# Kernel tuning notes

Hardware: AMD Instinct MI355X
Metric: run time of the kernel (lower is better)

## Reference

```python
import jax, jax.numpy as jnp
import numpy as np

PAD_IDX = 0  # y_vocab.token_to_idx('<PAD>'); source also hard-codes argmax==0 as stop
B, N, M, V, T = 8, 6, 64, 32000, 8  # N = max_span, T = template_len


def setup_inputs() -> dict:
    key = jax.random.key(0)
    k1, k2, k3 = jax.random.split(key, 3)
    input_decodings = jax.random.normal(k1, (B, N, M, V), dtype=jnp.float32)
    template = jax.random.uniform(k2, (B, T, N + 1), dtype=jnp.float32)
    spans = jax.random.randint(k3, (B,), 0, N)
    return {"input_decodings": input_decodings, "template": template, "spans": spans}


def reference(input_decodings, template, spans):
    Bq, Nq, Mq, Vq = input_decodings.shape
    Tq = template.shape[1]
    # original only reads template[i, t, :spans[i]+1]; zero out the rest
    span_mask = jnp.arange(Nq + 1)[None, None, :] <= spans[:, None, None]
    tmpl = jnp.where(span_mask, template, jnp.zeros((), template.dtype))
    # choices[b] = [pad_vector, flatten(input_decodings[b,0]), ..., flatten(input_decodings[b,N-1])]
    pad_vec = jnp.zeros((Mq * Vq,), input_decodings.dtype).at[PAD_IDX].set(1.0)
    choices = jnp.concatenate(
        [jnp.broadcast_to(pad_vec, (Bq, 1, Mq * Vq)), input_decodings.reshape(Bq, Nq, Mq * Vq)],
        axis=1,
    )  # [B, N+1, M*V]
    # all per-step template matmuls at once: [B, T, M, V]
    outputs = jnp.einsum('bts,bsd->btd', tmpl, choices).reshape(Bq, Tq, Mq, Vq)

    pos = jnp.arange(Mq)

    def step(carry, out_t):
        idx, result = carry  # idx: [B] int, result: [B, M, V]
        amax = jnp.argmax(out_t, axis=-1)  # [B, M]
        iszero = amax == 0
        # length of leading run of nonzero argmax (stop at first zero)
        out_len = jnp.where(jnp.any(iszero, axis=1), jnp.argmax(iszero, axis=1).astype(jnp.int32), Mq)
        out_len = jnp.minimum(out_len, Mq - idx)
        wmask = (pos[None, :] >= idx[:, None]) & (pos[None, :] < (idx + out_len)[:, None])  # [B, M]
        gather_idx = jnp.clip(pos[None, :] - idx[:, None], 0, Mq - 1)  # [B, M]
        src = jnp.take_along_axis(out_t, gather_idx[:, :, None], axis=1)  # [B, M, V]
        result = jnp.where(wmask[:, :, None], src, result)
        return (idx + out_len, result), None

    init = (jnp.zeros((Bq,), jnp.int32), jnp.zeros((Bq, Mq, Vq), input_decodings.dtype))
    (final_idx, result), _ = jax.lax.scan(step, init, jnp.swapaxes(outputs, 0, 1))
    return result
```

## Files before the change

### kernel.cpp

```cpp
#include <hip/hip_runtime.h>
#include <math.h>

namespace {
constexpr int kB = 8;
constexpr int kN = 6;
constexpr int kM = 64;
constexpr int kV = 32000;
constexpr int kT = 8;
constexpr int kS = kN + 1;
constexpr int kV4 = kV / 4;
constexpr int kThreads = 256;
}

__global__ void init_ws_kernel(int* __restrict__ len_raw) {
  int i = threadIdx.x;
  if (i < kB * kT) len_raw[i] = kM;
}

template <int NUSE>
__device__ __forceinline__ void pass1_body(const float* __restrict__ in,
                                           const float* __restrict__ tw,
                                           float* __restrict__ orow,
                                           int b, int m,
                                           int* __restrict__ len_raw) {
  const int tid = threadIdx.x;
  constexpr int NA = NUSE > 0 ? NUSE : 1;

  float w[kT][NA];
  float w0[kT];
#pragma unroll
  for (int t = 0; t < kT; ++t) {
    w0[t] = tw[t * kS];
#pragma unroll
    for (int n = 0; n < NUSE; ++n) w[t][n] = tw[t * kS + n + 1];
  }

  const float4* rows[NA];
#pragma unroll
  for (int n = 0; n < NUSE; ++n)
    rows[n] = (const float4*)(in + ((size_t)(b * kN + n) * kM + m) * kV);

  float mx[kT], v0[kT];
#pragma unroll
  for (int t = 0; t < kT; ++t) {
    mx[t] = -INFINITY;
    v0[t] = 0.0f;
  }

  for (int v4 = tid; v4 < kV4; v4 += kThreads) {
    float4 x[NA];
#pragma unroll
    for (int n = 0; n < NUSE; ++n) x[n] = rows[n][v4];
    const bool head = (v4 == 0);
#pragma unroll
    for (int t = 0; t < kT; ++t) {
      float ax = 0.0f, ay = 0.0f, az = 0.0f, aw = 0.0f;
#pragma unroll
      for (int n = 0; n < NUSE; ++n) {
        ax = fmaf(w[t][n], x[n].x, ax);
        ay = fmaf(w[t][n], x[n].y, ay);
        az = fmaf(w[t][n], x[n].z, az);
        aw = fmaf(w[t][n], x[n].w, aw);
      }
      if (head && m == 0) ax += w0[t];
      if (head) v0[t] = ax;
      mx[t] = fmaxf(mx[t], fmaxf(fmaxf(ax, ay), fmaxf(az, aw)));
      if (t == 0) ((float4*)orow)[v4] = make_float4(ax, ay, az, aw);
    }
  }

  __shared__ float red[kT][4];
  const int lane = tid & 63;
  const int wv = tid >> 6;
#pragma unroll
  for (int t = 0; t < kT; ++t) {
    float v = mx[t];
#pragma unroll
    for (int off = 32; off > 0; off >>= 1) v = fmaxf(v, __shfl_xor(v, off, 64));
    if (lane == 0) red[t][wv] = v;
  }
  __syncthreads();
  if (tid == 0) {
#pragma unroll
    for (int t = 0; t < kT; ++t) {
      float bm = fmaxf(fmaxf(red[t][0], red[t][1]), fmaxf(red[t][2], red[t][3]));
      if (v0[t] >= bm) atomicMin(&len_raw[b * kT + t], m);
    }
  }
}

__global__ __launch_bounds__(kThreads) void pass1_kernel(
    const float* __restrict__ in, const float* __restrict__ tmpl,
    const int* __restrict__ spans, float* __restrict__ out,
    int* __restrict__ len_raw) {
  const int blk = blockIdx.x;
  const int b = blk >> 6;
  const int m = blk & 63;
  int span = spans[b];
  int nuse = span < 0 ? 0 : (span > kN ? kN : span);
  const float* tw = tmpl + (size_t)b * kT * kS;
  float* orow = out + (size_t)(b * kM + m) * kV;
  switch (nuse) {
    case 0: pass1_body<0>(in, tw, orow, b, m, len_raw); break;
    case 1: pass1_body<1>(in, tw, orow, b, m, len_raw); break;
    case 2: pass1_body<2>(in, tw, orow, b, m, len_raw); break;
    case 3: pass1_body<3>(in, tw, orow, b, m, len_raw); break;
    case 4: pass1_body<4>(in, tw, orow, b, m, len_raw); break;
    case 5: pass1_body<5>(in, tw, orow, b, m, len_raw); break;
    case 6: pass1_body<6>(in, tw, orow, b, m, len_raw); break;
  }
}

__global__ void pass2_kernel(const int* __restrict__ len_raw,
                             int* __restrict__ sel) {
  int b = threadIdx.x;
  if (b >= kB) return;
  for (int m = 0; m < kM; ++m) sel[b * kM + m] = -1;
  int idx = 0;
  for (int t = 0; t < kT; ++t) {
    int L = len_raw[b * kT + t];
    if (L > kM - idx) L = kM - idx;
    for (int j = 0; j < L; ++j) sel[b * kM + idx + j] = t * 64 + j;
    idx += L;
  }
}

__global__ __launch_bounds__(kThreads) void pass3_kernel(
    const float* __restrict__ in, const float* __restrict__ tmpl,
    const int* __restrict__ spans, const int* __restrict__ sel,
    float* __restrict__ out) {
  const int blk = blockIdx.x;
  const int b = blk >> 6;
  const int m = blk & 63;
  const int s = sel[b * kM + m];
  if (s >= 0 && s < 64) return;

  const int tid = threadIdx.x;
  float* orow = out + (size_t)(b * kM + m) * kV;

  if (s < 0) {
    float4 z = make_float4(0.0f, 0.0f, 0.0f, 0.0f);
    for (int v4 = tid; v4 < kV4; v4 += kThreads) ((float4*)orow)[v4] = z;
    return;
  }

  const int t = s >> 6;
  const int row = s & 63;
  int span = spans[b];
  int nuse = span < 0 ? 0 : (span > kN ? kN : span);
  const float* tw = tmpl + ((size_t)b * kT + t) * kS;
  const float w0 = tw[0];
  float w[kN];
  for (int n = 0; n < kN; ++n) w[n] = (n < nuse) ? tw[n + 1] : 0.0f;

  const float4* rows[kN];
  for (int n = 0; n < kN; ++n)
    rows[n] = (const float4*)(in + ((size_t)(b * kN + n) * kM + row) * kV);

  for (int v4 = tid; v4 < kV4; v4 += kThreads) {
    float ax = 0.0f, ay = 0.0f, az = 0.0f, aw = 0.0f;
    for (int n = 0; n < nuse; ++n) {
      float4 x = rows[n][v4];
      ax = fmaf(w[n], x.x, ax);
      ay = fmaf(w[n], x.y, ay);
      az = fmaf(w[n], x.z, az);
      aw = fmaf(w[n], x.w, aw);
    }
    if (v4 == 0 && row == 0) ax += w0;
    ((float4*)orow)[v4] = make_float4(ax, ay, az, aw);
  }
}

extern "C" void kernel_launch(void* const* d_in, const int* in_sizes, int n_in,
                              void* d_out, int out_size, void* d_ws,
                              size_t ws_size, hipStream_t stream) {
  const float* in = (const float*)d_in[0];
  const float* tmpl = (const float*)d_in[1];
  const int* spans = (const int*)d_in[2];
  float* out = (float*)d_out;

  int* len_raw = (int*)d_ws;
  int* sel = len_raw + kB * kT;

  hipLaunchKernelGGL(init_ws_kernel, dim3(1), dim3(64), 0, stream, len_raw);
  hipLaunchKernelGGL(pass1_kernel, dim3(kB * kM), dim3(kThreads), 0, stream,
                     in, tmpl, spans, out, len_raw);
  hipLaunchKernelGGL(pass2_kernel, dim3(1), dim3(64), 0, stream, len_raw, sel);
  hipLaunchKernelGGL(pass3_kernel, dim3(kB * kM), dim3(kThreads), 0, stream,
                     in, tmpl, spans, sel, out);
}
```

Baseline: 506.6 us.

## Replace atomic length scan with per-row flags and merge selection into patch kernel

Pass 1 now writes a per-(batch, template step, row) flag instead of doing an atomicMin, so the init and serial pass2 kernels can be dropped. The patch kernel rebuilds each step's length with a wavefront ballot and recomputes the row selection per block. Loads and stores on the large activation and output streams become nontemporal to reduce cache pollution. This cuts two kernel launches and one serial kernel, at the cost of every patch block redundantly reading 512 flags.

```diff
diff --git a/kernel.cpp b/kernel.cpp
--- a/kernel.cpp
+++ b/kernel.cpp
@@ -12,17 +12,15 @@
 constexpr int kThreads = 256;
 }
 
-__global__ void init_ws_kernel(int* __restrict__ len_raw) {
-  int i = threadIdx.x;
-  if (i < kB * kT) len_raw[i] = kM;
-}
+typedef float f32x4 __attribute__((ext_vector_type(4)));
+
 
 template <int NUSE>
 __device__ __forceinline__ void pass1_body(const float* __restrict__ in,
                                            const float* __restrict__ tw,
                                            float* __restrict__ orow,
                                            int b, int m,
-                                           int* __restrict__ len_raw) {
+                                           int* __restrict__ flags) {
   const int tid = threadIdx.x;
   constexpr int NA = NUSE > 0 ? NUSE : 1;
 
@@ -35,10 +33,12 @@
     for (int n = 0; n < NUSE; ++n) w[t][n] = tw[t * kS + n + 1];
   }
 
-  const float4* rows[NA];
+  const f32x4* rows[NA];
 #pragma unroll
   for (int n = 0; n < NUSE; ++n)
-    rows[n] = (const float4*)(in + ((size_t)(b * kN + n) * kM + m) * kV);
+    rows[n] = (const f32x4*)(in + ((size_t)(b * kN + n) * kM + m) * kV);
+
+  f32x4* orow4 = (f32x4*)orow;
 
   float mx[kT], v0[kT];
 #pragma unroll
@@ -48,9 +48,9 @@
   }
 
   for (int v4 = tid; v4 < kV4; v4 += kThreads) {
-    float4 x[NA];
-#pragma unroll
-    for (int n = 0; n < NUSE; ++n) x[n] = rows[n][v4];
+    f32x4 x[NA];
+#pragma unroll
+    for (int n = 0; n < NUSE; ++n) x[n] = __builtin_nontemporal_load(&rows[n][v4]);
     const bool head = (v4 == 0);
 #pragma unroll
     for (int t = 0; t < kT; ++t) {
@@ -65,7 +65,10 @@
       if (head && m == 0) ax += w0[t];
       if (head) v0[t] = ax;
       mx[t] = fmaxf(mx[t], fmaxf(fmaxf(ax, ay), fmaxf(az, aw)));
-      if (t == 0) ((float4*)orow)[v4] = make_float4(ax, ay, az, aw);
+      if (t == 0) {
+        f32x4 o = {ax, ay, az, aw};
+        __builtin_nontemporal_store(o, &orow4[v4]);
+      }
     }
   }
 
@@ -84,7 +87,7 @@
 #pragma unroll
     for (int t = 0; t < kT; ++t) {
       float bm = fmaxf(fmaxf(red[t][0], red[t][1]), fmaxf(red[t][2], red[t][3]));
-      if (v0[t] >= bm) atomicMin(&len_raw[b * kT + t], m);
+      flags[(b * kT + t) * kM + m] = (v0[t] >= bm) ? 1 : 0;
     }
   }
 }
@@ -92,7 +95,7 @@
 __global__ __launch_bounds__(kThreads) void pass1_kernel(
     const float* __restrict__ in, const float* __restrict__ tmpl,
     const int* __restrict__ spans, float* __restrict__ out,
-    int* __restrict__ len_raw) {
+    int* __restrict__ flags) {
   const int blk = blockIdx.x;
   const int b = blk >> 6;
   const int m = blk & 63;
@@ -101,51 +104,63 @@
   const float* tw = tmpl + (size_t)b * kT * kS;
   float* orow = out + (size_t)(b * kM + m) * kV;
   switch (nuse) {
-    case 0: pass1_body<0>(in, tw, orow, b, m, len_raw); break;
-    case 1: pass1_body<1>(in, tw, orow, b, m, len_raw); break;
-    case 2: pass1_body<2>(in, tw, orow, b, m, len_raw); break;
-    case 3: pass1_body<3>(in, tw, orow, b, m, len_raw); break;
-    case 4: pass1_body<4>(in, tw, orow, b, m, len_raw); break;
-    case 5: pass1_body<5>(in, tw, orow, b, m, len_raw); break;
-    case 6: pass1_body<6>(in, tw, orow, b, m, len_raw); break;
-  }
-}
-
-__global__ void pass2_kernel(const int* __restrict__ len_raw,
-                             int* __restrict__ sel) {
-  int b = threadIdx.x;
-  if (b >= kB) return;
-  for (int m = 0; m < kM; ++m) sel[b * kM + m] = -1;
-  int idx = 0;
-  for (int t = 0; t < kT; ++t) {
-    int L = len_raw[b * kT + t];
-    if (L > kM - idx) L = kM - idx;
-    for (int j = 0; j < L; ++j) sel[b * kM + idx + j] = t * 64 + j;
-    idx += L;
-  }
-}
-
-__global__ __launch_bounds__(kThreads) void pass3_kernel(
+    case 0: pass1_body<0>(in, tw, orow, b, m, flags); break;
+    case 1: pass1_body<1>(in, tw, orow, b, m, flags); break;
+    case 2: pass1_body<2>(in, tw, orow, b, m, flags); break;
+    case 3: pass1_body<3>(in, tw, orow, b, m, flags); break;
+    case 4: pass1_body<4>(in, tw, orow, b, m, flags); break;
+    case 5: pass1_body<5>(in, tw, orow, b, m, flags); break;
+    case 6: pass1_body<6>(in, tw, orow, b, m, flags); break;
+  }
+}
+
+__global__ __launch_bounds__(kThreads) void patch_kernel(
     const float* __restrict__ in, const float* __restrict__ tmpl,
-    const int* __restrict__ spans, const int* __restrict__ sel,
+    const int* __restrict__ spans, const int* __restrict__ flags,
     float* __restrict__ out) {
   const int blk = blockIdx.x;
   const int b = blk >> 6;
   const int m = blk & 63;
-  const int s = sel[b * kM + m];
-  if (s >= 0 && s < 64) return;
-
   const int tid = threadIdx.x;
+  const int lane = tid & 63;
+
+  __shared__ int slen[kT];
+  if (tid < 64) {
+#pragma unroll
+    for (int t = 0; t < kT; ++t) {
+      int f = flags[(b * kT + t) * kM + lane];
+      unsigned long long bal = __ballot(f != 0);
+      if (lane == 0) slen[t] = bal ? (int)(__ffsll((long long)bal) - 1) : kM;
+    }
+  }
+  __syncthreads();
+
+  int sel_t = -1, sel_row = 0, idx = 0;
+#pragma unroll
+  for (int t = 0; t < kT; ++t) {
+    int L = slen[t];
+    if (L > kM - idx) L = kM - idx;
+    if (sel_t < 0 && m >= idx && m < idx + L) {
+      sel_t = t;
+      sel_row = m - idx;
+    }
+    idx += L;
+  }
+
+  if (sel_t == 0) return;
+
   float* orow = out + (size_t)(b * kM + m) * kV;
-
-  if (s < 0) {
-    float4 z = make_float4(0.0f, 0.0f, 0.0f, 0.0f);
-    for (int v4 = tid; v4 < kV4; v4 += kThreads) ((float4*)orow)[v4] = z;
+  f32x4* orow4 = (f32x4*)orow;
+
+  if (sel_t < 0) {
+    f32x4 z = {0.0f, 0.0f, 0.0f, 0.0f};
+    for (int v4 = tid; v4 < kV4; v4 += kThreads)
+      __builtin_nontemporal_store(z, &orow4[v4]);
     return;
   }
 
-  const int t = s >> 6;
-  const int row = s & 63;
+  const int t = sel_t;
+  const int row = sel_row;
   int span = spans[b];
   int nuse = span < 0 ? 0 : (span > kN ? kN : span);
   const float* tw = tmpl + ((size_t)b * kT + t) * kS;
@@ -153,21 +168,22 @@
   float w[kN];
   for (int n = 0; n < kN; ++n) w[n] = (n < nuse) ? tw[n + 1] : 0.0f;
 
-  const float4* rows[kN];
+  const f32x4* rows[kN];
   for (int n = 0; n < kN; ++n)
-    rows[n] = (const float4*)(in + ((size_t)(b * kN + n) * kM + row) * kV);
+    rows[n] = (const f32x4*)(in + ((size_t)(b * kN + n) * kM + row) * kV);
 
   for (int v4 = tid; v4 < kV4; v4 += kThreads) {
     float ax = 0.0f, ay = 0.0f, az = 0.0f, aw = 0.0f;
     for (int n = 0; n < nuse; ++n) {
-      float4 x = rows[n][v4];
+      f32x4 x = __builtin_nontemporal_load(&rows[n][v4]);
       ax = fmaf(w[n], x.x, ax);
       ay = fmaf(w[n], x.y, ay);
       az = fmaf(w[n], x.z, az);
       aw = fmaf(w[n], x.w, aw);
     }
     if (v4 == 0 && row == 0) ax += w0;
-    ((float4*)orow)[v4] = make_float4(ax, ay, az, aw);
+    f32x4 o = {ax, ay, az, aw};
+    __builtin_nontemporal_store(o, &orow4[v4]);
   }
 }
 
@@ -179,13 +195,10 @@
   const int* spans = (const int*)d_in[2];
   float* out = (float*)d_out;
 
-  int* len_raw = (int*)d_ws;
-  int* sel = len_raw + kB * kT;
-
-  hipLaunchKernelGGL(init_ws_kernel, dim3(1), dim3(64), 0, stream, len_raw);
+  int* flags = (int*)d_ws;
+
   hipLaunchKernelGGL(pass1_kernel, dim3(kB * kM), dim3(kThreads), 0, stream,
-                     in, tmpl, spans, out, len_raw);
-  hipLaunchKernelGGL(pass2_kernel, dim3(1), dim3(64), 0, stream, len_raw, sel);
-  hipLaunchKernelGGL(pass3_kernel, dim3(kB * kM), dim3(kThreads), 0, stream,
-                     in, tmpl, spans, sel, out);
-}
+                     in, tmpl, spans, out, flags);
+  hipLaunchKernelGGL(patch_kernel, dim3(kB * kM), dim3(kThreads), 0, stream,
+                     in, tmpl, spans, flags, out);
+}
```

Measured after the change: 485.5 us. 1.04x faster.
